# Kernel optimization log

Measured on AMD Instinct MI355X. Metric: run time of the kernel, lower is better.

The kernel has to match this reference:

```python
import jax, jax.numpy as jnp
import numpy as np

EPS = 1e-5  # GraphNorm eps


def setup_inputs() -> dict:
    key = jax.random.key(0)
    ks = jax.random.split(key, 8)
    B, N, D, L = 8, 2048, 128, 3
    return {
        "instance": jax.random.uniform(ks[0], (B, N, 2), jnp.float32),
        "Wn": jax.random.normal(ks[1], (D, 2), jnp.float32) * 0.5,
        "bn": jnp.zeros((D,), jnp.float32),
        "Wg": jax.random.normal(ks[2], (L, D, D), jnp.float32) / np.sqrt(D).astype(np.float32),
        "bg": jnp.zeros((L, D), jnp.float32),
        "gn_w": jnp.ones((D,), jnp.float32),
        "gn_b": jnp.zeros((D,), jnp.float32),
        "gn_a": jnp.ones((D,), jnp.float32),
    }


def reference(instance, Wn, bn, Wg, bg, gn_w, gn_b, gn_a):
    # instance: [B, N, 2] city coordinates. Graph is complete, so the PyG
    # edge-list GCN over all (i != j) pairs + self-loops is exactly a dense
    # symmetric-normalized adjacency matmul per graph.
    B, N, _ = instance.shape
    # pairwise Euclidean distances (cdist), safe sqrt to keep diagonal exact 0
    sq = jnp.sum(instance * instance, axis=-1)                      # [B, N]
    d2 = sq[:, :, None] + sq[:, None, :] - 2.0 * jnp.einsum(
        'bnd,bmd->bnm', instance, instance)                          # [B, N, N]
    pos = d2 > 0
    dist = jnp.where(pos, jnp.sqrt(jnp.where(pos, d2, 1.0)), 0.0)    # [B, N, N]
    # GCN edge weights = distances, self-loops added with weight 1.0
    A = dist + jnp.eye(N, dtype=dist.dtype)
    deg = jnp.sum(A, axis=-1)                                        # [B, N]
    dinv = jax.lax.rsqrt(deg)
    An = dinv[:, :, None] * A * dinv[:, None, :]                     # D^-1/2 A D^-1/2

    h = jnp.einsum('bne,de->bnd', instance, Wn) + bn                 # proj_node
    for l in range(Wg.shape[0]):
        # GCNConv: aggregate normalized messages of lin(x), then bias
        hw = jnp.einsum('bnm,bmd->bnd', An, jnp.einsum('bnd,ed->bne', h, Wg[l])) + bg[l]
        h = jnp.tanh(hw) + h                                         # activation + residual
        # GraphNorm (shared params across layers): per-graph, per-feature stats
        mean = jnp.mean(h, axis=1, keepdims=True)                    # [B, 1, D]
        sub = h - gn_a * mean
        var = jnp.mean(sub * sub, axis=1, keepdims=True)
        h = gn_w * sub * jax.lax.rsqrt(var + EPS) + gn_b
    return h  # [B, N, D] (unbatch+stack of equal-size graphs)
```

## Files before the change

kernel.cpp:

```cpp
#include <hip/hip_runtime.h>
#include <hip/hip_bf16.h>
#include <math.h>

#define BB 8
#define NN 2048
#define DD 128
#define LL 3
#define GN_EPS 1e-5f

typedef __attribute__((ext_vector_type(8))) short bf16x8;
typedef __attribute__((ext_vector_type(4))) float f32x4;
typedef __attribute__((ext_vector_type(8))) unsigned short u16x8;

#define FSQRT(x) __builtin_amdgcn_sqrtf(x)

__device__ __forceinline__ unsigned short f2bf(float f) {
    union { float f; unsigned u; } v; v.f = f;
    return (unsigned short)((v.u + 0x8000u) >> 16);
}

__device__ __forceinline__ float fast_tanh(float x) {
    float e = __expf(-2.0f * fabsf(x));
    float t = (1.0f - e) * __builtin_amdgcn_rcpf(1.0f + e);
    return copysignf(t, x);
}

__device__ __forceinline__ void stats_sc(float ps, float pq, float a, float w_,
                                         float b_, float& s, float& c) {
    const float inv_n = 1.0f / (float)NN;
    float mean = ps * inv_n;
    float msq  = pq * inv_n;
    float var  = msq - mean * mean * a * (2.0f - a);
    float rstd = rsqrtf(var + GN_EPS);
    s = w_ * rstd;
    c = b_ - s * (a * mean);
}


__global__ __launch_bounds__(256)
void prep_wg(const float* __restrict__ Wg, const float* __restrict__ Wn,
             const float* __restrict__ bn, unsigned short* __restrict__ wgf,
             float* __restrict__ weff, float* __restrict__ beff)
{
    const int f = blockIdx.x * 256 + threadIdx.x;
    const int l  = f >> 14;
    const int r  = f & 16383;
    const int dp = r >> 7;
    const int e  = r & 127;
    const int dpt = dp >> 4, ll = dp & 15;
    const int kc  = e >> 5,  eo = e & 31;
    wgf[((((l * 8 + dpt) * 4 + kc) * 16 + ll) << 5) + eo] = f2bf(Wg[f]);

    if (blockIdx.x == 0 && threadIdx.x < 128) {
        const int ee = threadIdx.x;
        float a0 = 0.f, a1 = 0.f, cc = 0.f;
        for (int d = 0; d < 128; ++d) {
            const float wv = Wg[ee * 128 + d];
            a0 = fmaf(wv, Wn[d * 2 + 0], a0);
            a1 = fmaf(wv, Wn[d * 2 + 1], a1);
            cc = fmaf(wv, bn[d], cc);
        }
        weff[ee * 2 + 0] = a0;
        weff[ee * 2 + 1] = a1;
        beff[ee] = cc;
    }
}

__global__ __launch_bounds__(256)
void gen_pack(const float* __restrict__ inst, const float* __restrict__ Wn,
              const float* __restrict__ bn, const float* __restrict__ weff,
              const float* __restrict__ beff,
              float* __restrict__ dinv, float* __restrict__ h,
              unsigned short* __restrict__ tp,
              float* __restrict__ psum, float* __restrict__ psq)
{
    __shared__ float cs[NN * 2];
    __shared__ float part[4][16];
    const int b     = blockIdx.x & 7;
    const int ntile = blockIdx.x >> 3;
    const int n0    = ntile * 16;
    const int tid   = threadIdx.x;
    const int w     = tid >> 6;
    const int lane  = tid & 63;
    const int lq    = lane >> 4;
    const int ll    = lane & 15;

    const float* instb = inst + b * NN * 2;
    for (int i = tid; i < (NN * 2) / 4; i += 256)
        ((float4*)cs)[i] = ((const float4*)instb)[i];
    __syncthreads();

    const int n = n0 + ll;
    const float nx = cs[n * 2 + 0];
    const float ny = cs[n * 2 + 1];

    const int diagkcg = ntile >> 1;
    float rs = 0.f;
    for (int kc = 0; kc < 16; ++kc) {
        const int kcg = w * 16 + kc;
        const int mb  = kcg * 32 + lq * 8;
        const float* cp = &cs[mb * 2];
        float4 c01 = *(const float4*)(cp + 0);
        float4 c23 = *(const float4*)(cp + 4);
        float4 c45 = *(const float4*)(cp + 8);
        float4 c67 = *(const float4*)(cp + 12);
        float mxx[8] = { c01.x, c01.z, c23.x, c23.z, c45.x, c45.z, c67.x, c67.z };
        float myy[8] = { c01.y, c01.w, c23.y, c23.w, c45.y, c45.w, c67.y, c67.w };
        float dist[8];
        #pragma unroll
        for (int j = 0; j < 8; ++j) {
            float dx = nx - mxx[j];
            float dy = ny - myy[j];
            dist[j] = FSQRT(dx * dx + dy * dy);
        }
        if (kcg == diagkcg) {
            #pragma unroll
            for (int j = 0; j < 8; ++j)
                if (mb + j == n) dist[j] = 1.0f;
        }
        #pragma unroll
        for (int j = 0; j < 8; ++j) rs += dist[j];
    }

    rs += __shfl_xor(rs, 16);
    rs += __shfl_xor(rs, 32);
    if (lq == 0) part[w][ll] = rs;
    __syncthreads();
    if (tid < 16)
        dinv[b * NN + n0 + tid] = rsqrtf(part[0][tid] + part[1][tid] +
                                         part[2][tid] + part[3][tid]);

    {
        const int d  = tid & 127;
        const int r0 = tid >> 7;
        const float w0 = Wn[d * 2 + 0];
        const float w1 = Wn[d * 2 + 1];
        const float bv = bn[d];
        const float we0 = weff[d * 2 + 0];
        const float we1 = weff[d * 2 + 1];
        const float be  = beff[d];
        const int kcg   = ntile >> 1;
        const int mbase = (ntile & 1) * 16;
        const int dt    = d >> 4;
        const int lld   = d & 15;
        unsigned short* tpd =
            tp + (((size_t)(b * 64 + kcg) * 8 + dt) * 64 + lld) * 8;
        #pragma unroll
        for (int r = r0; r < 16; r += 2) {
            const float x0 = cs[(n0 + r) * 2 + 0];
            const float x1 = cs[(n0 + r) * 2 + 1];
            h[((size_t)b * NN + n0 + r) * DD + d] = fmaf(x0, w0, fmaf(x1, w1, bv));
            const float dv = rsqrtf(part[0][r] + part[1][r] + part[2][r] + part[3][r]);
            const int mloc = mbase + r;
            const int lqa  = mloc >> 3;
            const int j    = mloc & 7;
            tpd[(size_t)lqa * 128 + j] = f2bf(dv * fmaf(x0, we0, fmaf(x1, we1, be)));
        }
    }
    if (blockIdx.x == 0) {
        for (int i = tid; i < LL * BB * DD; i += 256) { psum[i] = 0.f; psq[i] = 0.f; }
    }
}

template <bool HP>
__global__ __launch_bounds__(256)
void lin_mfma(const float* __restrict__ h, const unsigned short* __restrict__ wgf_l,
              const float* __restrict__ dinv,
              const float* __restrict__ psumP, const float* __restrict__ psqP,
              const float* __restrict__ ga, const float* __restrict__ gw,
              const float* __restrict__ gb, unsigned short* __restrict__ tp)
{
    __shared__ float sL[DD], cL[DD];
    const int tid  = threadIdx.x;
    const int b    = blockIdx.x & 7;
    const int tile = blockIdx.x >> 3;
    const int row0 = b * NN + tile * 32;
    const int w    = tid >> 6;
    const int lane = tid & 63;
    const int lq   = lane >> 4;
    const int ll   = lane & 15;

    if (tid < DD) {
        float s = 1.0f, c = 0.0f;
        if (HP)
            stats_sc(psumP[b * DD + tid], psqP[b * DD + tid],
                     ga[tid], gw[tid], gb[tid], s, c);
        sL[tid] = s; cL[tid] = c;
    }
    __syncthreads();

    bf16x8 aw[2][4];
    #pragma unroll
    for (int mt = 0; mt < 2; ++mt) {
        const int dpt = 2 * w + mt;
        #pragma unroll
        for (int kc = 0; kc < 4; ++kc)
            aw[mt][kc] = *(const bf16x8*)&wgf_l[(((dpt * 4 + kc) * 16 + ll) << 5) + lq * 8];
    }

    bf16x8 bh[2][4];
    #pragma unroll
    for (int nt = 0; nt < 2; ++nt) {
        const float* hrow = h + (size_t)(row0 + nt * 16 + ll) * DD;
        #pragma unroll
        for (int kc = 0; kc < 4; ++kc) {
            float4 h0 = *(const float4*)&hrow[kc * 32 + lq * 8];
            float4 h1 = *(const float4*)&hrow[kc * 32 + lq * 8 + 4];
            const int e0 = kc * 32 + lq * 8;
            bf16x8 p;
            p[0] = (short)f2bf(fmaf(sL[e0 + 0], h0.x, cL[e0 + 0]));
            p[1] = (short)f2bf(fmaf(sL[e0 + 1], h0.y, cL[e0 + 1]));
            p[2] = (short)f2bf(fmaf(sL[e0 + 2], h0.z, cL[e0 + 2]));
            p[3] = (short)f2bf(fmaf(sL[e0 + 3], h0.w, cL[e0 + 3]));
            p[4] = (short)f2bf(fmaf(sL[e0 + 4], h1.x, cL[e0 + 4]));
            p[5] = (short)f2bf(fmaf(sL[e0 + 5], h1.y, cL[e0 + 5]));
            p[6] = (short)f2bf(fmaf(sL[e0 + 6], h1.z, cL[e0 + 6]));
            p[7] = (short)f2bf(fmaf(sL[e0 + 7], h1.w, cL[e0 + 7]));
            bh[nt][kc] = p;
        }
    }

    f32x4 acc[2][2];
    #pragma unroll
    for (int i = 0; i < 2; ++i)
        #pragma unroll
        for (int j = 0; j < 2; ++j) acc[i][j] = (f32x4)0.0f;

    #pragma unroll
    for (int kc = 0; kc < 4; ++kc)
        #pragma unroll
        for (int nt = 0; nt < 2; ++nt)
            #pragma unroll
            for (int mt = 0; mt < 2; ++mt)
                acc[nt][mt] = __builtin_amdgcn_mfma_f32_16x16x32_bf16(
                    bh[nt][kc], aw[mt][kc], acc[nt][mt], 0, 0, 0);

    #pragma unroll
    for (int nt = 0; nt < 2; ++nt) {
        const int mloc0 = nt * 16 + lq * 4;
        const int lq_a  = mloc0 >> 3;
        const int j0    = mloc0 & 7;
        float4 di4 = *(const float4*)&dinv[row0 + mloc0];
        #pragma unroll
        for (int mt = 0; mt < 2; ++mt) {
            const int dt = 2 * w + mt;
            ushort4 pk;
            pk.x = f2bf(acc[nt][mt][0] * di4.x);
            pk.y = f2bf(acc[nt][mt][1] * di4.y);
            pk.z = f2bf(acc[nt][mt][2] * di4.z);
            pk.w = f2bf(acc[nt][mt][3] * di4.w);
            *(ushort4*)&tp[((size_t)((b * 64 + tile) * 8 + dt) * 64 + lq_a * 16 + ll) * 8 + j0] = pk;
        }
    }
}

template <bool HP>
__global__ __launch_bounds__(256, 2)
void agg_mfma(const float* __restrict__ inst, const unsigned short* __restrict__ tp,
              const float* __restrict__ dinv, const float* __restrict__ bg_l,
              const float* __restrict__ psumP, const float* __restrict__ psqP,
              const float* __restrict__ ga, const float* __restrict__ gw,
              const float* __restrict__ gb,
              float* __restrict__ h, float* __restrict__ psum, float* __restrict__ psq)
{
    __shared__ float cs[NN * 2];
    __shared__ char Abuf[2][8192];
    const int b    = blockIdx.x & 7;
    const int t2   = blockIdx.x >> 3;
    const int n0   = t2 * 32;
    const int tid  = threadIdx.x;
    const int w    = tid >> 6;
    const int lane = tid & 63;
    const int lq   = lane >> 4;
    const int ll   = lane & 15;

    const float* instb = inst + b * NN * 2;
    for (int i = tid; i < (NN * 2) / 4; i += 256)
        ((float4*)cs)[i] = ((const float4*)instb)[i];

    const unsigned short* tpb = tp + ((size_t)b * 64 * 8) * 512 + lane * 8;

    f32x4 acc[2][2];
    acc[0][0] = (f32x4)0.0f; acc[0][1] = (f32x4)0.0f;
    acc[1][0] = (f32x4)0.0f; acc[1][1] = (f32x4)0.0f;

    bf16x8 fb[2][2][4];

    __syncthreads();

    const int ntw  = w >> 1;
    const int s0w  = (w & 1) * 2;
    const int nw   = n0 + ntw * 16 + ll;
    const float nxw = cs[nw * 2 + 0];
    const float nyw = cs[nw * 2 + 1];
    const int diagkcg = (n0 + ntw * 16) >> 5;

#define MKFRAGS(kk) { \
        char* wb = &Abuf[(kk) & 1][0]; \
        _Pragma("unroll") \
        for (int si = 0; si < 2; ++si) { \
            const int s_   = s0w + si; \
            const int kcg_ = (kk) * 4 + s_; \
            const int mb_  = kcg_ * 32 + lq * 8; \
            const float* cp_ = &cs[mb_ * 2]; \
            float4 c01 = *(const float4*)(cp_ + 0); \
            float4 c23 = *(const float4*)(cp_ + 4); \
            float4 c45 = *(const float4*)(cp_ + 8); \
            float4 c67 = *(const float4*)(cp_ + 12); \
            float mxx[8] = { c01.x, c01.z, c23.x, c23.z, c45.x, c45.z, c67.x, c67.z }; \
            float myy[8] = { c01.y, c01.w, c23.y, c23.w, c45.y, c45.w, c67.y, c67.w }; \
            u16x8 pk; \
            _Pragma("unroll") \
            for (int j = 0; j < 8; ++j) { \
                float dx = nxw - mxx[j]; \
                float dy = nyw - myy[j]; \
                float dv = FSQRT(dx * dx + dy * dy); \
                if (kcg_ == diagkcg && mb_ + j == nw) dv = 1.0f; \
                pk[j] = f2bf(dv); \
            } \
            *(u16x8*)(wb + (2 * w + si) * 1024 + lane * 16) = pk; \
        } \
    }
#define LOADB(c) { \
        const int kb_ = (c) * 4; \
        _Pragma("unroll") \
        for (int s_ = 0; s_ < 4; ++s_) { \
            fb[(c) & 1][0][s_] = *(const bf16x8*)(tpb + (size_t)((kb_ + s_) * 8 + 2 * w + 0) * 512); \
            fb[(c) & 1][1][s_] = *(const bf16x8*)(tpb + (size_t)((kb_ + s_) * 8 + 2 * w + 1) * 512); \
        } \
    }

    MKFRAGS(0)
    LOADB(0)
    __syncthreads();

    #pragma unroll
    for (int k = 0; k < 16; ++k) {
        bf16x8 af[2][4];
        const char* lb = &Abuf[k & 1][0];
        #pragma unroll
        for (int nt = 0; nt < 2; ++nt)
            #pragma unroll
            for (int s = 0; s < 4; ++s)
                af[nt][s] = *(const bf16x8*)(lb + (nt * 4 + s) * 1024 + lane * 16);
        if (k < 15) {
            LOADB(k + 1)
            MKFRAGS(k + 1)
        }
        #pragma unroll
        for (int s = 0; s < 4; ++s)
            #pragma unroll
            for (int nt = 0; nt < 2; ++nt) {
                acc[nt][0] = __builtin_amdgcn_mfma_f32_16x16x32_bf16(fb[k & 1][0][s], af[nt][s], acc[nt][0], 0, 0, 0);
                acc[nt][1] = __builtin_amdgcn_mfma_f32_16x16x32_bf16(fb[k & 1][1][s], af[nt][s], acc[nt][1], 0, 0, 0);
            }
        __syncthreads();
    }
#undef MKFRAGS
#undef LOADB

    const float di0 = dinv[b * NN + n0 + ll];
    const float di1 = dinv[b * NN + n0 + 16 + ll];
    #pragma unroll
    for (int dtl = 0; dtl < 2; ++dtl) {
        const int d0 = (2 * w + dtl) * 16 + lq * 4;
        float4 bg4 = *(const float4*)&bg_l[d0];
        float sres[4] = {1.f, 1.f, 1.f, 1.f}, cres[4] = {0.f, 0.f, 0.f, 0.f};
        if (HP) {
            float4 ps4 = *(const float4*)&psumP[b * DD + d0];
            float4 pq4 = *(const float4*)&psqP[b * DD + d0];
            float4 ga4 = *(const float4*)&ga[d0];
            float4 gw4 = *(const float4*)&gw[d0];
            float4 gb4 = *(const float4*)&gb[d0];
            stats_sc(ps4.x, pq4.x, ga4.x, gw4.x, gb4.x, sres[0], cres[0]);
            stats_sc(ps4.y, pq4.y, ga4.y, gw4.y, gb4.y, sres[1], cres[1]);
            stats_sc(ps4.z, pq4.z, ga4.z, gw4.z, gb4.z, sres[2], cres[2]);
            stats_sc(ps4.w, pq4.w, ga4.w, gw4.w, gb4.w, sres[3], cres[3]);
        }
        float hs[4] = {0.f, 0.f, 0.f, 0.f}, hq[4] = {0.f, 0.f, 0.f, 0.f};
        #pragma unroll
        for (int nt = 0; nt < 2; ++nt) {
            const int n = n0 + nt * 16 + ll;
            const float di = nt ? di1 : di0;
            size_t idx = ((size_t)b * NN + n) * DD + d0;
            float4 hv = *(const float4*)&h[idx];
            float outv[4];
            #pragma unroll
            for (int r = 0; r < 4; ++r) {
                float pre = di * acc[nt][dtl][r] + (&bg4.x)[r];
                outv[r] = fast_tanh(pre) + fmaf(sres[r], (&hv.x)[r], cres[r]);
                hs[r] += outv[r];
                hq[r] += outv[r] * outv[r];
            }
            float4 ov = { outv[0], outv[1], outv[2], outv[3] };
            *(float4*)&h[idx] = ov;
        }

        #pragma unroll
        for (int off = 1; off < 16; off <<= 1) {
            #pragma unroll
            for (int r = 0; r < 4; ++r) {
                hs[r] += __shfl_xor(hs[r], off);
                hq[r] += __shfl_xor(hq[r], off);
            }
        }
        if (ll == 0) {
            #pragma unroll
            for (int r = 0; r < 4; ++r) {
                atomicAdd(&psum[b * DD + d0 + r], hs[r]);
                atomicAdd(&psq[b * DD + d0 + r], hq[r]);
            }
        }
    }
}

__global__ __launch_bounds__(256)
void apply_kernel(const float* __restrict__ h,
                  const float* __restrict__ psum2, const float* __restrict__ psq2,
                  const float* __restrict__ ga, const float* __restrict__ gw,
                  const float* __restrict__ gb, float* __restrict__ dst)
{
    const int i4 = blockIdx.x * 256 + threadIdx.x;
    const int dg = (i4 & 31) * 4;
    const int b  = i4 >> 16;
    float4 hv = ((const float4*)h)[i4];
    float o[4];
    #pragma unroll
    for (int j = 0; j < 4; ++j) {
        const int d = dg + j;
        float s, c;
        stats_sc(psum2[b * DD + d], psq2[b * DD + d], ga[d], gw[d], gb[d], s, c);
        o[j] = fmaf(s, (&hv.x)[j], c);
    }
    float4 ov = { o[0], o[1], o[2], o[3] };
    ((float4*)dst)[i4] = ov;
}

extern "C" void kernel_launch(void* const* d_in, const int* in_sizes, int n_in,
                              void* d_out, int out_size, void* d_ws, size_t ws_size,
                              hipStream_t stream)
{
    const float* inst = (const float*)d_in[0];
    const float* Wn   = (const float*)d_in[1];
    const float* bn   = (const float*)d_in[2];
    const float* Wg   = (const float*)d_in[3];
    const float* bg   = (const float*)d_in[4];
    const float* gw   = (const float*)d_in[5];
    const float* gb   = (const float*)d_in[6];
    const float* ga   = (const float*)d_in[7];
    float* out = (float*)d_out;

    float* ws   = (float*)d_ws;
    float* dinv = ws;
    float* h    = dinv + BB * NN;
    float* psum = h + (size_t)BB * NN * DD;
    float* psq  = psum + LL * BB * DD;
    float* weff = psq + LL * BB * DD;
    float* beff = weff + 2 * DD;
    unsigned short* wgf = (unsigned short*)(beff + DD);
    unsigned short* tp  = wgf + LL * DD * DD;

    prep_wg<<<(LL * DD * DD) / 256, 256, 0, stream>>>(Wg, Wn, bn, wgf, weff, beff);
    gen_pack<<<1024, 256, 0, stream>>>(inst, Wn, bn, weff, beff, dinv, h, tp, psum, psq);

    agg_mfma<false><<<512, 256, 0, stream>>>(
        inst, tp, dinv, bg + 0 * DD, nullptr, nullptr, ga, gw, gb, h, psum, psq);

    for (int l = 1; l < LL; ++l) {
        const unsigned short* wgl = wgf + (size_t)l * DD * DD;
        const float* psP = psum + (size_t)(l - 1) * BB * DD;
        const float* pqP = psq  + (size_t)(l - 1) * BB * DD;
        float* psL = psum + (size_t)l * BB * DD;
        float* pqL = psq  + (size_t)l * BB * DD;
        lin_mfma<true><<<(BB * NN) / 32, 256, 0, stream>>>(
            h, wgl, dinv, psP, pqP, ga, gw, gb, tp);
        agg_mfma<true><<<512, 256, 0, stream>>>(
            inst, tp, dinv, bg + l * DD, psP, pqP, ga, gw, gb, h, psL, pqL);
    }
    apply_kernel<<<(BB * NN * DD / 4) / 256, 256, 0, stream>>>(
        h, psum + 2 * BB * DD, psq + 2 * BB * DD, ga, gw, gb, out);
}
```

Measured before the change: 189.9 us.

## Build distance fragments in two large LDS phases instead of per-step double buffer

Replaces the per-iteration double-buffered LDS distance-fragment generation with two phases. Each phase computes 32 k-chunks of bf16 distance fragments into a 64 KB LDS buffer, with each wave handling both row tiles. Then 8 MFMA steps run with only one barrier per phase, which removes most __syncthreads calls and reuses loaded coordinates for two rows. In exchange, LDS use per block rises sharply (16 KB cs + 64 KB Abuf), which likely cuts occupancy below the launch_bounds target of 2 blocks/CU. Distance math also no longer overlaps with MFMA.

```diff
diff --git a/kernel.cpp b/kernel.cpp
--- a/kernel.cpp
+++ b/kernel.cpp
@@ -264,7 +264,7 @@
               float* __restrict__ h, float* __restrict__ psum, float* __restrict__ psq)
 {
     __shared__ float cs[NN * 2];
-    __shared__ char Abuf[2][8192];
+    __shared__ char Abuf[64 * 1024];
     const int b    = blockIdx.x & 7;
     const int t2   = blockIdx.x >> 3;
     const int n0   = t2 * 32;
@@ -288,39 +288,11 @@
 
     __syncthreads();
 
-    const int ntw  = w >> 1;
-    const int s0w  = (w & 1) * 2;
-    const int nw   = n0 + ntw * 16 + ll;
-    const float nxw = cs[nw * 2 + 0];
-    const float nyw = cs[nw * 2 + 1];
-    const int diagkcg = (n0 + ntw * 16) >> 5;
-
-#define MKFRAGS(kk) { \
-        char* wb = &Abuf[(kk) & 1][0]; \
-        _Pragma("unroll") \
-        for (int si = 0; si < 2; ++si) { \
-            const int s_   = s0w + si; \
-            const int kcg_ = (kk) * 4 + s_; \
-            const int mb_  = kcg_ * 32 + lq * 8; \
-            const float* cp_ = &cs[mb_ * 2]; \
-            float4 c01 = *(const float4*)(cp_ + 0); \
-            float4 c23 = *(const float4*)(cp_ + 4); \
-            float4 c45 = *(const float4*)(cp_ + 8); \
-            float4 c67 = *(const float4*)(cp_ + 12); \
-            float mxx[8] = { c01.x, c01.z, c23.x, c23.z, c45.x, c45.z, c67.x, c67.z }; \
-            float myy[8] = { c01.y, c01.w, c23.y, c23.w, c45.y, c45.w, c67.y, c67.w }; \
-            u16x8 pk; \
-            _Pragma("unroll") \
-            for (int j = 0; j < 8; ++j) { \
-                float dx = nxw - mxx[j]; \
-                float dy = nyw - myy[j]; \
-                float dv = FSQRT(dx * dx + dy * dy); \
-                if (kcg_ == diagkcg && mb_ + j == nw) dv = 1.0f; \
-                pk[j] = f2bf(dv); \
-            } \
-            *(u16x8*)(wb + (2 * w + si) * 1024 + lane * 16) = pk; \
-        } \
-    }
+    const int   nr0 = n0 + ll;
+    const int   nr1 = n0 + 16 + ll;
+    const float nx0 = cs[nr0 * 2 + 0], ny0 = cs[nr0 * 2 + 1];
+    const float nx1 = cs[nr1 * 2 + 0], ny1 = cs[nr1 * 2 + 1];
+
 #define LOADB(c) { \
         const int kb_ = (c) * 4; \
         _Pragma("unroll") \
@@ -330,33 +302,62 @@
         } \
     }
 
-    MKFRAGS(0)
     LOADB(0)
-    __syncthreads();
-
-    #pragma unroll
-    for (int k = 0; k < 16; ++k) {
-        bf16x8 af[2][4];
-        const char* lb = &Abuf[k & 1][0];
-        #pragma unroll
-        for (int nt = 0; nt < 2; ++nt)
+
+    #pragma unroll
+    for (int ph = 0; ph < 2; ++ph) {
+        #pragma unroll
+        for (int q = 0; q < 8; ++q) {
+            const int kcg = ph * 32 + w * 8 + q;
+            const int mb  = kcg * 32 + lq * 8;
+            const float* cp = &cs[mb * 2];
+            float4 c01 = *(const float4*)(cp + 0);
+            float4 c23 = *(const float4*)(cp + 4);
+            float4 c45 = *(const float4*)(cp + 8);
+            float4 c67 = *(const float4*)(cp + 12);
+            float mxx[8] = { c01.x, c01.z, c23.x, c23.z, c45.x, c45.z, c67.x, c67.z };
+            float myy[8] = { c01.y, c01.w, c23.y, c23.w, c45.y, c45.w, c67.y, c67.w };
+            const int slot0 = (2 * w + (q >> 2)) * 8 + (q & 3);
+            const bool dk = (kcg == t2);
+            u16x8 pk0, pk1;
+            #pragma unroll
+            for (int j = 0; j < 8; ++j) {
+                float dx0 = nx0 - mxx[j], dy0 = ny0 - myy[j];
+                float dv0 = FSQRT(dx0 * dx0 + dy0 * dy0);
+                if (dk && mb + j == nr0) dv0 = 1.0f;
+                pk0[j] = f2bf(dv0);
+                float dx1 = nx1 - mxx[j], dy1 = ny1 - myy[j];
+                float dv1 = FSQRT(dx1 * dx1 + dy1 * dy1);
+                if (dk && mb + j == nr1) dv1 = 1.0f;
+                pk1[j] = f2bf(dv1);
+            }
+            *(u16x8*)(Abuf + (slot0 + 0) * 1024 + lane * 16) = pk0;
+            *(u16x8*)(Abuf + (slot0 + 4) * 1024 + lane * 16) = pk1;
+        }
+        __syncthreads();
+
+        #pragma unroll
+        for (int i = 0; i < 8; ++i) {
+            const int k = ph * 8 + i;
+            bf16x8 af[2][4];
+            #pragma unroll
+            for (int nt = 0; nt < 2; ++nt)
+                #pragma unroll
+                for (int s = 0; s < 4; ++s)
+                    af[nt][s] = *(const bf16x8*)(Abuf + ((i * 8 + nt * 4 + s) * 1024) + lane * 16);
+            if (k < 15) {
+                LOADB(k + 1)
+            }
             #pragma unroll
             for (int s = 0; s < 4; ++s)
-                af[nt][s] = *(const bf16x8*)(lb + (nt * 4 + s) * 1024 + lane * 16);
-        if (k < 15) {
-            LOADB(k + 1)
-            MKFRAGS(k + 1)
-        }
-        #pragma unroll
-        for (int s = 0; s < 4; ++s)
-            #pragma unroll
-            for (int nt = 0; nt < 2; ++nt) {
-                acc[nt][0] = __builtin_amdgcn_mfma_f32_16x16x32_bf16(fb[k & 1][0][s], af[nt][s], acc[nt][0], 0, 0, 0);
-                acc[nt][1] = __builtin_amdgcn_mfma_f32_16x16x32_bf16(fb[k & 1][1][s], af[nt][s], acc[nt][1], 0, 0, 0);
-            }
+                #pragma unroll
+                for (int nt = 0; nt < 2; ++nt) {
+                    acc[nt][0] = __builtin_amdgcn_mfma_f32_16x16x32_bf16(fb[k & 1][0][s], af[nt][s], acc[nt][0], 0, 0, 0);
+                    acc[nt][1] = __builtin_amdgcn_mfma_f32_16x16x32_bf16(fb[k & 1][1][s], af[nt][s], acc[nt][1], 0, 0, 0);
+                }
+        }
         __syncthreads();
     }
-#undef MKFRAGS
 #undef LOADB
 
     const float di0 = dinv[b * NN + n0 + ll];
```

After: 199.9 us. 1.05x slower.

## Generate distance tiles in two large phases instead of per-step double buffering

Applied to the files above, without the earlier changes.

The aggregation kernel now builds half of the on-the-fly distance A-fragments (8 k-steps) into a 64KB LDS buffer at once, then runs 8 MFMA steps with no barriers in between, instead of double-buffering one k-step at a time with a barrier after each step. Each wave computes distances for both row tiles per column chunk. This is meant to cut per-step __syncthreads overhead and let the MFMA loop run uninterrupted, at the cost of much larger LDS use (96KB with the coordinate cache), which may limit the kernel to one block per CU, and of serialising distance generation with the MFMA work.

```diff
diff --git a/kernel.cpp b/kernel.cpp
--- a/kernel.cpp
+++ b/kernel.cpp
@@ -264,7 +264,7 @@
               float* __restrict__ h, float* __restrict__ psum, float* __restrict__ psq)
 {
     __shared__ float cs[NN * 2];
-    __shared__ char Abuf[2][8192];
+    __shared__ char Abuf[64 * 1024];
     const int b    = blockIdx.x & 7;
     const int t2   = blockIdx.x >> 3;
     const int n0   = t2 * 32;
@@ -284,80 +284,100 @@
     acc[0][0] = (f32x4)0.0f; acc[0][1] = (f32x4)0.0f;
     acc[1][0] = (f32x4)0.0f; acc[1][1] = (f32x4)0.0f;
 
-    bf16x8 fb[2][2][4];
-
-    __syncthreads();
-
-    const int ntw  = w >> 1;
-    const int s0w  = (w & 1) * 2;
-    const int nw   = n0 + ntw * 16 + ll;
-    const float nxw = cs[nw * 2 + 0];
-    const float nyw = cs[nw * 2 + 1];
-    const int diagkcg = (n0 + ntw * 16) >> 5;
-
-#define MKFRAGS(kk) { \
-        char* wb = &Abuf[(kk) & 1][0]; \
+    bf16x8 fbA0[4], fbA1[4], fbB0[4], fbB1[4];
+
+    __syncthreads();
+
+    const int   nr0 = n0 + ll;
+    const int   nr1 = n0 + 16 + ll;
+    const float nx0 = cs[nr0 * 2 + 0], ny0 = cs[nr0 * 2 + 1];
+    const float nx1 = cs[nr1 * 2 + 0], ny1 = cs[nr1 * 2 + 1];
+
+#define LOADB_INTO(B0, B1, KK) { \
         _Pragma("unroll") \
-        for (int si = 0; si < 2; ++si) { \
-            const int s_   = s0w + si; \
-            const int kcg_ = (kk) * 4 + s_; \
-            const int mb_  = kcg_ * 32 + lq * 8; \
-            const float* cp_ = &cs[mb_ * 2]; \
-            float4 c01 = *(const float4*)(cp_ + 0); \
-            float4 c23 = *(const float4*)(cp_ + 4); \
-            float4 c45 = *(const float4*)(cp_ + 8); \
-            float4 c67 = *(const float4*)(cp_ + 12); \
+        for (int s_ = 0; s_ < 4; ++s_) { \
+            B0[s_] = *(const bf16x8*)(tpb + (size_t)(((KK) * 4 + s_) * 8 + 2 * w + 0) * 512); \
+            B1[s_] = *(const bf16x8*)(tpb + (size_t)(((KK) * 4 + s_) * 8 + 2 * w + 1) * 512); \
+        } \
+    }
+
+#define GENPH(PH) { \
+        _Pragma("unroll") \
+        for (int q = 0; q < 8; ++q) { \
+            const int kcg = (PH) * 32 + w * 8 + q; \
+            const int mb  = kcg * 32 + lq * 8; \
+            const float* cp = &cs[mb * 2]; \
+            float4 c01 = *(const float4*)(cp + 0); \
+            float4 c23 = *(const float4*)(cp + 4); \
+            float4 c45 = *(const float4*)(cp + 8); \
+            float4 c67 = *(const float4*)(cp + 12); \
             float mxx[8] = { c01.x, c01.z, c23.x, c23.z, c45.x, c45.z, c67.x, c67.z }; \
             float myy[8] = { c01.y, c01.w, c23.y, c23.w, c45.y, c45.w, c67.y, c67.w }; \
-            u16x8 pk; \
+            const int slot0 = (2 * w + (q >> 2)) * 8 + (q & 3); \
+            const bool dk = (kcg == t2); \
+            u16x8 pk0, pk1; \
             _Pragma("unroll") \
             for (int j = 0; j < 8; ++j) { \
-                float dx = nxw - mxx[j]; \
-                float dy = nyw - myy[j]; \
-                float dv = FSQRT(dx * dx + dy * dy); \
-                if (kcg_ == diagkcg && mb_ + j == nw) dv = 1.0f; \
-                pk[j] = f2bf(dv); \
+                float dx0 = nx0 - mxx[j], dy0 = ny0 - myy[j]; \
+                float dv0 = FSQRT(dx0 * dx0 + dy0 * dy0); \
+                if (dk && mb + j == nr0) dv0 = 1.0f; \
+                pk0[j] = f2bf(dv0); \
+                float dx1 = nx1 - mxx[j], dy1 = ny1 - myy[j]; \
+                float dv1 = FSQRT(dx1 * dx1 + dy1 * dy1); \
+                if (dk && mb + j == nr1) dv1 = 1.0f; \
+                pk1[j] = f2bf(dv1); \
             } \
-            *(u16x8*)(wb + (2 * w + si) * 1024 + lane * 16) = pk; \
+            *(u16x8*)(Abuf + (slot0 + 0) * 1024 + lane * 16) = pk0; \
+            *(u16x8*)(Abuf + (slot0 + 4) * 1024 + lane * 16) = pk1; \
         } \
     }
-#define LOADB(c) { \
-        const int kb_ = (c) * 4; \
+
+#define STEP(I, C0, C1, DOLOAD, N0, N1, KN) { \
+        bf16x8 af[2][4]; \
         _Pragma("unroll") \
-        for (int s_ = 0; s_ < 4; ++s_) { \
-            fb[(c) & 1][0][s_] = *(const bf16x8*)(tpb + (size_t)((kb_ + s_) * 8 + 2 * w + 0) * 512); \
-            fb[(c) & 1][1][s_] = *(const bf16x8*)(tpb + (size_t)((kb_ + s_) * 8 + 2 * w + 1) * 512); \
-        } \
-    }
-
-    MKFRAGS(0)
-    LOADB(0)
-    __syncthreads();
-
-    #pragma unroll
-    for (int k = 0; k < 16; ++k) {
-        bf16x8 af[2][4];
-        const char* lb = &Abuf[k & 1][0];
-        #pragma unroll
-        for (int nt = 0; nt < 2; ++nt)
-            #pragma unroll
-            for (int s = 0; s < 4; ++s)
-                af[nt][s] = *(const bf16x8*)(lb + (nt * 4 + s) * 1024 + lane * 16);
-        if (k < 15) {
-            LOADB(k + 1)
-            MKFRAGS(k + 1)
-        }
-        #pragma unroll
-        for (int s = 0; s < 4; ++s)
-            #pragma unroll
-            for (int nt = 0; nt < 2; ++nt) {
-                acc[nt][0] = __builtin_amdgcn_mfma_f32_16x16x32_bf16(fb[k & 1][0][s], af[nt][s], acc[nt][0], 0, 0, 0);
-                acc[nt][1] = __builtin_amdgcn_mfma_f32_16x16x32_bf16(fb[k & 1][1][s], af[nt][s], acc[nt][1], 0, 0, 0);
-            }
-        __syncthreads();
-    }
-#undef MKFRAGS
-#undef LOADB
+        for (int nt = 0; nt < 2; ++nt) \
+            _Pragma("unroll") \
+            for (int s = 0; s < 4; ++s) \
+                af[nt][s] = *(const bf16x8*)(Abuf + (((I) * 8 + nt * 4 + s) * 1024) + lane * 16); \
+        if (DOLOAD) LOADB_INTO(N0, N1, KN) \
+        _Pragma("unroll") \
+        for (int s = 0; s < 4; ++s) \
+            _Pragma("unroll") \
+            for (int nt = 0; nt < 2; ++nt) { \
+                acc[nt][0] = __builtin_amdgcn_mfma_f32_16x16x32_bf16(C0[s], af[nt][s], acc[nt][0], 0, 0, 0); \
+                acc[nt][1] = __builtin_amdgcn_mfma_f32_16x16x32_bf16(C1[s], af[nt][s], acc[nt][1], 0, 0, 0); \
+            } \
+    }
+
+    LOADB_INTO(fbA0, fbA1, 0)
+
+    GENPH(0)
+    __syncthreads();
+    STEP(0, fbA0, fbA1, true,  fbB0, fbB1, 1)
+    STEP(1, fbB0, fbB1, true,  fbA0, fbA1, 2)
+    STEP(2, fbA0, fbA1, true,  fbB0, fbB1, 3)
+    STEP(3, fbB0, fbB1, true,  fbA0, fbA1, 4)
+    STEP(4, fbA0, fbA1, true,  fbB0, fbB1, 5)
+    STEP(5, fbB0, fbB1, true,  fbA0, fbA1, 6)
+    STEP(6, fbA0, fbA1, true,  fbB0, fbB1, 7)
+    STEP(7, fbB0, fbB1, true,  fbA0, fbA1, 8)
+    __syncthreads();
+
+    GENPH(1)
+    __syncthreads();
+    STEP(0, fbA0, fbA1, true,  fbB0, fbB1, 9)
+    STEP(1, fbB0, fbB1, true,  fbA0, fbA1, 10)
+    STEP(2, fbA0, fbA1, true,  fbB0, fbB1, 11)
+    STEP(3, fbB0, fbB1, true,  fbA0, fbA1, 12)
+    STEP(4, fbA0, fbA1, true,  fbB0, fbB1, 13)
+    STEP(5, fbB0, fbB1, true,  fbA0, fbA1, 14)
+    STEP(6, fbA0, fbA1, true,  fbB0, fbB1, 15)
+    STEP(7, fbB0, fbB1, false, fbA0, fbA1, 0)
+    __syncthreads();
+
+#undef STEP
+#undef GENPH
+#undef LOADB_INTO
 
     const float di0 = dinv[b * NN + n0 + ll];
     const float di1 = dinv[b * NN + n0 + 16 + ll];
```

Result: slower. 198.9 us (+4.7%).
